# Optimization experiments

Measured on AMD Instinct MI355X. Metric: run time of the kernel, lower is better.

Reference implementation:

```python
import jax, jax.numpy as jnp
import numpy as np

B, L, D, H, T = 1024, 50, 4, 512, 30


def _lstm_cell(x, h, c, W_ih, W_hh, b_ih, b_hh):
    # PyTorch LSTM gate order: i, f, g, o
    g = x @ W_ih.T + b_ih + h @ W_hh.T + b_hh
    i, f, gg, o = jnp.split(g, 4, axis=-1)
    c = jax.nn.sigmoid(f) * c + jax.nn.sigmoid(i) * jnp.tanh(gg)
    h = jax.nn.sigmoid(o) * jnp.tanh(c)
    return h, c


def setup_inputs() -> dict:
    key = jax.random.key(0)
    ks = jax.random.split(key, 16)
    s = 0.05
    return {
        "input_tensor": jax.random.normal(ks[0], (B, L, D), jnp.float32),
        "target_len": T,
        "enc_W_ih": jax.random.normal(ks[1], (4 * H, D), jnp.float32) * s,
        "enc_W_hh": jax.random.normal(ks[2], (4 * H, H), jnp.float32) * s,
        "enc_b_ih": jax.random.normal(ks[3], (4 * H,), jnp.float32) * s,
        "enc_b_hh": jax.random.normal(ks[4], (4 * H,), jnp.float32) * s,
        "attn_W": jax.random.normal(ks[5], (L, H + D), jnp.float32) * s,
        "attn_b": jax.random.normal(ks[6], (L,), jnp.float32) * s,
        "comb_W": jax.random.normal(ks[7], (H, H + D), jnp.float32) * s,
        "comb_b": jax.random.normal(ks[8], (H,), jnp.float32) * s,
        "dec_W_ih": jax.random.normal(ks[9], (4 * H, H), jnp.float32) * s,
        "dec_W_hh": jax.random.normal(ks[10], (4 * H, H), jnp.float32) * s,
        "dec_b_ih": jax.random.normal(ks[11], (4 * H,), jnp.float32) * s,
        "dec_b_hh": jax.random.normal(ks[12], (4 * H,), jnp.float32) * s,
        "out_W": jax.random.normal(ks[13], (D, H), jnp.float32) * s,
        "out_b": jax.random.normal(ks[14], (D,), jnp.float32) * s,
    }


def reference(input_tensor, target_len, enc_W_ih, enc_W_hh, enc_b_ih, enc_b_hh,
              attn_W, attn_b, comb_W, comb_b,
              dec_W_ih, dec_W_hh, dec_b_ih, dec_b_hh, out_W, out_b):
    b = input_tensor.shape[0]

    # ---- encoder LSTM over input_len steps ----
    def enc_step(carry, x_t):
        h, c = carry
        h, c = _lstm_cell(x_t, h, c, enc_W_ih, enc_W_hh, enc_b_ih, enc_b_hh)
        return (h, c), h

    h0 = jnp.zeros((b, H), input_tensor.dtype)
    (h_enc, c_enc), enc_hs = jax.lax.scan(enc_step, (h0, h0),
                                          jnp.swapaxes(input_tensor, 0, 1))
    encoder_outputs = jnp.swapaxes(enc_hs, 0, 1)  # [B, L, H]

    # ---- recursive attention decoder over target_len steps ----
    def dec_step(carry, _):
        h, c, x = carry
        # faithful to torch: h.reshape(h.shape[1], -1).transpose(1, 0)
        h_r = jnp.transpose(h.reshape(H, -1))  # [B, H] (memory reinterpret)
        attn_logits = jnp.concatenate([x, h_r], axis=1) @ attn_W.T + attn_b
        attn_weights = jax.nn.softmax(attn_logits, axis=1)        # [B, L]
        attn_applied = jnp.einsum('bl,blh->bh', attn_weights, encoder_outputs)
        comb = jnp.concatenate([x, attn_applied], axis=1) @ comb_W.T + comb_b
        comb = jax.nn.relu(comb)                                  # [B, H]
        h, c = _lstm_cell(comb, h, c, dec_W_ih, dec_W_hh, dec_b_ih, dec_b_hh)
        pred = h @ out_W.T + out_b                                # [B, D]
        return (h, c, pred), pred

    dec_in0 = input_tensor[:, -1, :]
    _, preds = jax.lax.scan(dec_step, (h_enc, c_enc, dec_in0), None,
                            length=target_len)
    return jnp.swapaxes(preds, 0, 1)  # [B, target_len, D]
```

## Files before the change

kernel.cpp:

```cpp
#include <hip/hip_runtime.h>
#include <hip/hip_bf16.h>

#define Bsz   1024
#define Lseq  50
#define Din   4
#define Hd    512
#define Tlen  30
#define NWG   256

typedef __hip_bfloat16 bf16;
typedef short s16x8 __attribute__((ext_vector_type(8)));
typedef short s16x4 __attribute__((ext_vector_type(4)));
typedef float f32x4 __attribute__((ext_vector_type(4)));
typedef int   i32x2 __attribute__((ext_vector_type(2)));

__device__ __forceinline__ float bf2f(bf16 x){ return __bfloat162float(x); }
__device__ __forceinline__ bf16  f2bf(float x){ return __float2bfloat16(x); }
__device__ __forceinline__ float bfbits2f(short u){
    union { unsigned int ui; float f; } v;
    v.ui = ((unsigned int)(unsigned short)u) << 16;
    return v.f;
}
__device__ __forceinline__ short f2bfbits(float x){
    bf16 h = f2bf(x); short s; __builtin_memcpy(&s, &h, 2); return s;
}
__device__ __forceinline__ float sigm(float x){ return 1.0f/(1.0f + __expf(-x)); }
__device__ __forceinline__ float ftanh(float x){
    const float e = __expf(2.0f*x);
    return 1.0f - 2.0f/(e + 1.0f);
}
__device__ __forceinline__ i32x2 pack4(float a, float b, float c, float d){
    i32x2 v;
    v[0] = (int)(unsigned short)f2bfbits(a) | ((int)(unsigned short)f2bfbits(b) << 16);
    v[1] = (int)(unsigned short)f2bfbits(c) | ((int)(unsigned short)f2bfbits(d) << 16);
    return v;
}

#define OFF_ABUF0   (0u)
#define OFF_ABUF1   (2u<<20)
#define OFF_ATTNAP  (8u<<20)
#define OFF_XDEC    (9u<<20)
#define OFF_FLAG    ((9u<<20) + (16u<<10))
#define OFF_COMBWR  ((9u<<20) + (32u<<10))
#define OFF_ATTNWR  ((9u<<20) + (600u<<10))
#define OFF_FLAGS   ((9u<<20) + (704u<<10))
#define OFF_WCACHE  (10u<<20)
#define OFF_ENCOUT  (18u<<20)

#define WC_INPUT 0
#define WC_EWIH  204800
#define WC_EWHH  212992
#define WC_EBIH  1261568
#define WC_EBHH  1263616
#define WC_AW    1265664
#define WC_AB    1291464
#define WC_CW    1291520
#define WC_CB    1555712
#define WC_DWIH  1556224
#define WC_DWHH  2604800
#define WC_DBIH  3653376
#define WC_DBHH  3655424
#define WC_OW    3657472
#define WC_OB    3659520
#define WC_TOTAL 3659524

__device__ __constant__ int WOFF[15] = {
    WC_INPUT, WC_EWIH, WC_EWHH, WC_EBIH, WC_EBHH, WC_AW, WC_AB, WC_CW,
    WC_CB, WC_DWIH, WC_DWHH, WC_DBIH, WC_DBHH, WC_OW, WC_OB };
__device__ __constant__ int WNUM[15] = {
    204800, 8192, 1048576, 2048, 2048, 25800, 50, 264192,
    512, 1048576, 1048576, 2048, 2048, 2048, 4 };

struct Ptrs15 { const void* p[15]; };

__global__ void probe_kernel(const unsigned int* __restrict__ w, int* flag){
    __shared__ int cnt;
    if (threadIdx.x == 0) cnt = 0;
    __syncthreads();
    int c = 0;
    for (int i = threadIdx.x; i < 4096; i += 256){
        unsigned e = (w[i] >> 7) & 0xFFu;
        c += (e >= 0x80u) ? 1 : 0;
    }
    atomicAdd(&cnt, c);
    __syncthreads();
    if (threadIdx.x == 0) *flag = (cnt > 400) ? 1 : 0;
}

__global__ __launch_bounds__(256) void convert_kernel(
    Ptrs15 srcs, const int* __restrict__ flag, bf16* __restrict__ dst)
{
    const int f = *flag;
    for (int idx = blockIdx.x*256 + threadIdx.x; idx < WC_TOTAL;
         idx += gridDim.x*256){
        int a = 0;
#pragma unroll
        for (int j = 1; j < 15; ++j) if (idx >= WOFF[j]) a = j;
        const int local = idx - WOFF[a];
        if (local >= WNUM[a]) continue;
        bf16 v;
        if (f) v = f2bf(((const float*)srcs.p[a])[local]);
        else   v = ((const bf16*)srcs.p[a])[local];
        dst[idx] = v;
    }
}

__global__ __launch_bounds__(256) void setup_kernel(
    bf16* __restrict__ Abuf0, bf16* __restrict__ Abuf1,
    bf16* __restrict__ combWr, bf16* __restrict__ attnWr,
    const bf16* __restrict__ cWc, const bf16* __restrict__ aWc)
{
    const unsigned idx = blockIdx.x*256u + threadIdx.x;
    if (idx < (unsigned)Bsz*Hd){
        const unsigned row = idx >> 9, col = idx & (Hd-1);
        const bf16 z = f2bf(0.0f);
        Abuf0[(size_t)row*1024 + Hd + col] = z;
        Abuf1[(size_t)row*1024 + Hd + col] = z;
    }
    if (idx < (unsigned)Hd*Hd)
        combWr[idx] = cWc[(size_t)(idx >> 9)*(Hd+Din) + Din + (idx & (Hd-1))];
    if (idx < (unsigned)Lseq*Hd)
        attnWr[idx] = aWc[(size_t)(idx >> 9)*(Hd+Din) + Din + (idx & (Hd-1))];
}

struct MegaP {
    const bf16 *input, *eWih, *eWhh, *ebih, *ebhh;
    const bf16 *aW, *ab, *cW, *cb, *dWih, *dWhh, *dbih, *dbhh, *oW, *ob;
    const bf16 *combWr, *attnWr;
    bf16 *A0, *A1, *encout, *attnap, *xdec;
    int *wflag, *gflag, *xccmap;
    const int *flag;
    void *dout;
};

__global__ __launch_bounds__(512, 2) void mega_kernel(MegaP P)
{
    __shared__ short whh_lds[128*536];
    __shared__ short hr_s[4][Hd];
    __shared__ float ctx_s[2][4][8][64];
    __shared__ float aw_s[4][64];
    __shared__ int   xmap_s[NWG];
    __shared__ int   info_s[2];

    const int wg = blockIdx.x, tid = threadIdx.x;
    const int wave = tid >> 6, lane = tid & 63;
    const int quad = lane >> 4, l15 = lane & 15;
    const int lbase = lane & ~3;
    const int f32out = *P.flag;

    const int grp = wg & 7, rank = wg >> 3;

    int ep = 0;

    auto flag_round = [&](bool fence){
        ++ep;
        __syncthreads();
        if (tid == 0){
            if (fence) __threadfence();
            __hip_atomic_store(P.wflag + wg*16, ep, __ATOMIC_RELAXED, __HIP_MEMORY_SCOPE_SYSTEM);
        }
        if (rank == 0){
            if (tid < 32){
                int* f = P.wflag + (tid*8 + grp)*16;
                while (__hip_atomic_load(f, __ATOMIC_RELAXED, __HIP_MEMORY_SCOPE_SYSTEM) < ep)
                    __builtin_amdgcn_s_sleep(1);
            }
            __syncthreads();
            if (tid == 0)
                __hip_atomic_store(P.gflag + grp*16, ep, __ATOMIC_RELAXED, __HIP_MEMORY_SCOPE_SYSTEM);
        }
        if (tid < 8){
            int* f = P.gflag + tid*16;
            while (__hip_atomic_load(f, __ATOMIC_RELAXED, __HIP_MEMORY_SCOPE_SYSTEM) < ep)
                __builtin_amdgcn_s_sleep(1);
        }
        __syncthreads();
    };

    auto GSYNC = [&](){
        flag_round(true);
        asm volatile("buffer_inv sc0 sc1" ::: "memory");
        __syncthreads();
        flag_round(false);
    };

    auto XSYNC = [&](int balv){
        if (!balv){ GSYNC(); return; }
        ++ep;
        __syncthreads();
        if (tid == 0)
            __hip_atomic_store(P.wflag + wg*16, ep, __ATOMIC_RELAXED, __HIP_MEMORY_SCOPE_SYSTEM);
        if (tid < 32){
            int* f = P.wflag + (tid*8 + grp)*16;
            while (__hip_atomic_load(f, __ATOMIC_RELAXED, __HIP_MEMORY_SCOPE_SYSTEM) < ep)
                __builtin_amdgcn_s_sleep(1);
        }
        __syncthreads();
        asm volatile("buffer_inv" ::: "memory");
    };

    if (tid == 0){
        int xcc = 0;
        asm volatile("s_getreg_b32 %0, hwreg(HW_REG_XCC_ID)" : "=s"(xcc));
        P.xccmap[wg] = xcc & 7;
    }
    GSYNC();
    if (tid < NWG) xmap_s[tid] = P.xccmap[tid];
    __syncthreads();
    if (tid == 0){
        int ok = 1;
        for (int g = 0; g < 8; ++g){
            const int x0 = xmap_s[g];
            for (int i = 1; i < 32; ++i) ok &= (xmap_s[i*8 + g] == x0);
        }
        info_s[0] = ok;
    }
    __syncthreads();
    const int bal = info_s[0];

    bf16* bufs[2] = { P.A0, P.A1 };

    const int mt = grp*2 + (rank >> 4), nt = rank & 15;
    const int bm0 = mt << 6, hc0 = nt << 5;
    const int wm = wave >> 2, wn = wave & 3;
    const int arow0 = bm0 + wm*32 + l15;

    int ng[2];
#pragma unroll
    for (int nf = 0; nf < 2; ++nf){
        const int n = wn*32 + nf*16 + l15;
        ng[nf] = (n & 3)*Hd + hc0 + (n >> 2);
    }

    float bias_e[2], wxv_e[2][4];
#pragma unroll
    for (int nf = 0; nf < 2; ++nf){
        bias_e[nf] = bf2f(P.ebih[ng[nf]]) + bf2f(P.ebhh[ng[nf]]);
        const s16x4 t4 = *reinterpret_cast<const s16x4*>(P.eWih + (size_t)ng[nf]*Din);
#pragma unroll
        for (int d = 0; d < 4; ++d) wxv_e[nf][d] = bfbits2f(t4[d]);
    }

    s16x8 breg[2][16];
#pragma unroll
    for (int nf = 0; nf < 2; ++nf)
#pragma unroll
        for (int sl = 0; sl < 16; ++sl)
            breg[nf][sl] = *reinterpret_cast<const s16x8*>(
                P.eWhh + (size_t)ng[nf]*Hd + sl*32 + quad*8);

    float creg[2][2][4];
#pragma unroll
    for (int a = 0; a < 2; ++a)
#pragma unroll
        for (int b = 0; b < 2; ++b)
#pragma unroll
            for (int r = 0; r < 4; ++r) creg[a][b][r] = 0.0f;

    for (int t = 0; t < Lseq; ++t){
        const bf16* Ain = bufs[t&1] + Hd;
        bf16* hout = bufs[(t+1)&1] + Hd;

        f32x4 acc[2][2];
#pragma unroll
        for (int mf=0; mf<2; ++mf)
#pragma unroll
            for (int nf=0; nf<2; ++nf) acc[mf][nf] = (f32x4)0.0f;

        s16x8 afr[2];
#pragma unroll
        for (int sl = 0; sl < 16; ++sl){
#pragma unroll
            for (int mf = 0; mf < 2; ++mf)
                afr[mf] = *reinterpret_cast<const s16x8*>(
                    Ain + (size_t)(arow0 + mf*16)*1024 + sl*32 + quad*8);
#pragma unroll
            for (int mf = 0; mf < 2; ++mf)
#pragma unroll
                for (int nf = 0; nf < 2; ++nf)
                    acc[mf][nf] = __builtin_amdgcn_mfma_f32_16x16x32_bf16(
                        afr[mf], breg[nf][sl], acc[mf][nf], 0, 0, 0);
        }

#pragma unroll
        for (int mf = 0; mf < 2; ++mf){
#pragma unroll
            for (int r = 0; r < 4; ++r){
                const int m = bm0 + wm*32 + mf*16 + quad*4 + r;
                const s16x4 xt = *reinterpret_cast<const s16x4*>(
                    P.input + ((size_t)m*Lseq + t)*Din);
                float xv[4];
#pragma unroll
                for (int d = 0; d < 4; ++d) xv[d] = bfbits2f(xt[d]);
#pragma unroll
                for (int nf = 0; nf < 2; ++nf){
                    const int n_loc = wn*32 + nf*16 + l15;
                    float gv = acc[mf][nf][r] + bias_e[nf]
                             + xv[0]*wxv_e[nf][0] + xv[1]*wxv_e[nf][1]
                             + xv[2]*wxv_e[nf][2] + xv[3]*wxv_e[nf][3];
                    const float gi = __shfl(gv, lbase+0);
                    const float gf = __shfl(gv, lbase+1);
                    const float gg = __shfl(gv, lbase+2);
                    const float go = __shfl(gv, lbase+3);
                    if ((lane & 3) == 0){
                        const int hcol = hc0 + (n_loc >> 2);
                        const float cn = sigm(gf)*creg[mf][nf][r] + sigm(gi)*ftanh(gg);
                        creg[mf][nf][r] = cn;
                        const float hv = sigm(go)*ftanh(cn);
                        const bf16 hb = f2bf(hv);
                        hout[(size_t)m*1024 + hcol] = hb;
                        P.encout[((size_t)m*Lseq + t)*Hd + hcol] = hb;
                    }
                }
            }
        }
        if (t == Lseq-1) GSYNC(); else XSYNC(bal);
    }

#pragma unroll
    for (int nf = 0; nf < 2; ++nf)
#pragma unroll
        for (int sl = 0; sl < 16; ++sl)
            breg[nf][sl] = *reinterpret_cast<const s16x8*>(
                P.dWih + (size_t)ng[nf]*Hd + sl*32 + quad*8);

    float bias_d[2];
#pragma unroll
    for (int nf = 0; nf < 2; ++nf)
        bias_d[nf] = bf2f(P.dbih[ng[nf]]) + bf2f(P.dbhh[ng[nf]]);

    for (int i = tid; i < 128*64; i += 512){
        const int col = i >> 6;
        const int k8  = (i & 63) * 8;
        const int g   = (col & 3)*Hd + hc0 + (col >> 2);
        const s16x8 v = *reinterpret_cast<const s16x8*>(P.dWhh + (size_t)g*Hd + k8);
        *reinterpret_cast<s16x8*>(&whh_lds[col*536 + k8]) = v;
    }

    const int b0 = grp*128 + rank*4;
    const int s_uni = b0 >> 9;
    const int p0 = b0 & (Hd-1);

    const int cwm = wave >> 1, cwn = wave & 1;
    const int ccol = hc0 + cwn*16 + l15;
    float bias_c, wxv_c[4];
    {
        bias_c = bf2f(P.cb[ccol]);
        const s16x4 t4 = *reinterpret_cast<const s16x4*>(P.cW + (size_t)ccol*(Hd+Din));
#pragma unroll
        for (int d = 0; d < 4; ++d) wxv_c[d] = bfbits2f(t4[d]);
    }
    __syncthreads();

    for (int t = 0; t < Tlen; ++t){
        const int p = t & 1;
        const bf16* hprev = bufs[p] + Hd;

        {
            const s16x4 hv = *reinterpret_cast<const s16x4*>(
                hprev + (size_t)(2*tid + s_uni)*1024 + p0);
            hr_s[0][tid] = hv[0]; hr_s[1][tid] = hv[1];
            hr_s[2][tid] = hv[2]; hr_s[3][tid] = hv[3];
        }
        __syncthreads();

        if (wave < 4){
            const int b = b0 + wave;
            float x0, x1, x2, x3;
            if (t == 0){
                const bf16* xp = P.input + ((size_t)b*Lseq + (Lseq-1))*Din;
                x0 = bf2f(xp[0]); x1 = bf2f(xp[1]); x2 = bf2f(xp[2]); x3 = bf2f(xp[3]);
            } else {
                float q0=0.f, q1=0.f, q2=0.f, q3=0.f;
                const bf16* hb = hprev + (size_t)b*1024;
                for (int k = lane; k < Hd; k += 64){
                    const float hv = bf2f(hb[k]);
                    q0 += hv*bf2f(P.oW[k]);
                    q1 += hv*bf2f(P.oW[Hd+k]);
                    q2 += hv*bf2f(P.oW[2*Hd+k]);
                    q3 += hv*bf2f(P.oW[3*Hd+k]);
                }
#pragma unroll
                for (int off = 32; off; off >>= 1){
                    q0 += __shfl_down(q0, off); q1 += __shfl_down(q1, off);
                    q2 += __shfl_down(q2, off); q3 += __shfl_down(q3, off);
                }
                x0 = __shfl(q0,0) + bf2f(P.ob[0]);
                x1 = __shfl(q1,0) + bf2f(P.ob[1]);
                x2 = __shfl(q2,0) + bf2f(P.ob[2]);
                x3 = __shfl(q3,0) + bf2f(P.ob[3]);
                if (lane == 0){
                    const size_t o = ((size_t)b*Tlen + (t-1))*Din;
                    if (f32out){
                        float* dp = (float*)P.dout + o;
                        dp[0]=x0; dp[1]=x1; dp[2]=x2; dp[3]=x3;
                    } else {
                        *reinterpret_cast<i32x2*>((bf16*)P.dout + o) = pack4(x0,x1,x2,x3);
                    }
                }
            }
            if (lane == 0)
                *reinterpret_cast<i32x2*>(P.xdec + (size_t)b*Din) = pack4(x0,x1,x2,x3);

            float logit = -3.0e38f;
            if (lane < Lseq){
                float a0 = bf2f(P.ab[lane]);
                {
                    const bf16* wx = P.aW + (size_t)lane*(Hd+Din);
                    a0 += x0*bf2f(wx[0]) + x1*bf2f(wx[1]) + x2*bf2f(wx[2]) + x3*bf2f(wx[3]);
                }
                float a1 = 0.f, a2 = 0.f, a3 = 0.f;
                const bf16* wr = P.attnWr + (size_t)lane*Hd;
                for (int j = 0; j < Hd; j += 16){
                    float t4[4] = {0.f,0.f,0.f,0.f};
#pragma unroll
                    for (int q = 0; q < 4; ++q){
                        const s16x4 hw = *reinterpret_cast<const s16x4*>(&hr_s[wave][j + q*4]);
                        const s16x4 wv = *reinterpret_cast<const s16x4*>(wr + j + q*4);
                        t4[q] = bfbits2f(hw[0])*bfbits2f(wv[0]) + bfbits2f(hw[1])*bfbits2f(wv[1])
                              + bfbits2f(hw[2])*bfbits2f(wv[2]) + bfbits2f(hw[3])*bfbits2f(wv[3]);
                    }
                    a0 += t4[0]; a1 += t4[1]; a2 += t4[2]; a3 += t4[3];
                }
                logit = (a0 + a1) + (a2 + a3);
            }
            float mx = logit;
#pragma unroll
            for (int off = 32; off; off >>= 1) mx = fmaxf(mx, __shfl_xor(mx, off));
            const float e = (lane < Lseq) ? __expf(logit - mx) : 0.0f;
            float se = e;
#pragma unroll
            for (int off = 32; off; off >>= 1) se += __shfl_xor(se, off);
            aw_s[wave][lane] = e / se;
        }
        __syncthreads();

        {
            const int r = wave & 3, half = wave >> 2;
            const int b = b0 + r;
            float acc8[8] = {0.f,0.f,0.f,0.f,0.f,0.f,0.f,0.f};
            const bf16* eb = P.encout + (size_t)b*Lseq*Hd + lane*8;
            for (int i = 0; i < 25; ++i){
                const int l = half*25 + i;
                const float w = aw_s[r][l];
                const s16x8 ch = *reinterpret_cast<const s16x8*>(eb + (size_t)l*Hd);
#pragma unroll
                for (int q = 0; q < 8; ++q) acc8[q] += w * bfbits2f(ch[q]);
            }
#pragma unroll
            for (int q = 0; q < 8; ++q) ctx_s[half][r][q][lane] = acc8[q];
        }
        __syncthreads();

        if (wave < 4){
            const int b = b0 + wave;
            s16x8 ov;
#pragma unroll
            for (int q = 0; q < 8; ++q)
                ov[q] = f2bfbits(ctx_s[0][wave][q][lane] + ctx_s[1][wave][q][lane]);
            *reinterpret_cast<s16x8*>(P.attnap + (size_t)b*Hd + lane*8) = ov;
        }
        XSYNC(bal);

        {
            f32x4 cacc = (f32x4)0.0f;
            const bf16* Ab = P.attnap + (size_t)(bm0 + cwm*16 + l15)*Hd + quad*8;
#pragma unroll
            for (int kk = 0; kk < 16; ++kk){
                const s16x8 bfr = *reinterpret_cast<const s16x8*>(
                    P.combWr + (size_t)ccol*Hd + kk*32 + quad*8);
                const s16x8 afr2 = *reinterpret_cast<const s16x8*>(Ab + kk*32);
                cacc = __builtin_amdgcn_mfma_f32_16x16x32_bf16(afr2, bfr, cacc, 0, 0, 0);
            }
            bf16* outp = bufs[p];
#pragma unroll
            for (int r = 0; r < 4; ++r){
                const int m = bm0 + cwm*16 + quad*4 + r;
                const s16x4 xt = *reinterpret_cast<const s16x4*>(P.xdec + (size_t)m*Din);
                float v = cacc[r] + bias_c
                        + bfbits2f(xt[0])*wxv_c[0] + bfbits2f(xt[1])*wxv_c[1]
                        + bfbits2f(xt[2])*wxv_c[2] + bfbits2f(xt[3])*wxv_c[3];
                v = fmaxf(v, 0.0f);
                outp[(size_t)m*1024 + ccol] = f2bf(v);
            }
        }
        XSYNC(bal);

        {
            const bf16* Ain = bufs[p];
            bf16* hout = bufs[p^1] + Hd;
            f32x4 acc[2][2];
#pragma unroll
            for (int mf=0; mf<2; ++mf)
#pragma unroll
                for (int nf=0; nf<2; ++nf) acc[mf][nf] = (f32x4)0.0f;

            s16x8 afr[2], bfr[2];
#pragma unroll
            for (int sl = 0; sl < 16; ++sl){
#pragma unroll
                for (int mf = 0; mf < 2; ++mf)
                    afr[mf] = *reinterpret_cast<const s16x8*>(
                        Ain + (size_t)(arow0 + mf*16)*1024 + sl*32 + quad*8);
#pragma unroll
                for (int mf = 0; mf < 2; ++mf)
#pragma unroll
                    for (int nf = 0; nf < 2; ++nf)
                        acc[mf][nf] = __builtin_amdgcn_mfma_f32_16x16x32_bf16(
                            afr[mf], breg[nf][sl], acc[mf][nf], 0, 0, 0);
            }
#pragma unroll
            for (int sl = 0; sl < 16; ++sl){
#pragma unroll
                for (int nf = 0; nf < 2; ++nf){
                    const int nl = wn*32 + nf*16 + l15;
                    bfr[nf] = *reinterpret_cast<const s16x8*>(
                        &whh_lds[nl*536 + sl*32 + quad*8]);
                }
#pragma unroll
                for (int mf = 0; mf < 2; ++mf)
                    afr[mf] = *reinterpret_cast<const s16x8*>(
                        Ain + (size_t)(arow0 + mf*16)*1024 + Hd + sl*32 + quad*8);
#pragma unroll
                for (int mf = 0; mf < 2; ++mf)
#pragma unroll
                    for (int nf = 0; nf < 2; ++nf)
                        acc[mf][nf] = __builtin_amdgcn_mfma_f32_16x16x32_bf16(
                            afr[mf], bfr[nf], acc[mf][nf], 0, 0, 0);
            }

#pragma unroll
            for (int mf = 0; mf < 2; ++mf){
#pragma unroll
                for (int r = 0; r < 4; ++r){
                    const int m = bm0 + wm*32 + mf*16 + quad*4 + r;
#pragma unroll
                    for (int nf = 0; nf < 2; ++nf){
                        const int n_loc = wn*32 + nf*16 + l15;
                        float gv = acc[mf][nf][r] + bias_d[nf];
                        const float gi = __shfl(gv, lbase+0);
                        const float gf = __shfl(gv, lbase+1);
                        const float gg = __shfl(gv, lbase+2);
                        const float go = __shfl(gv, lbase+3);
                        if ((lane & 3) == 0){
                            const int hcol = hc0 + (n_loc >> 2);
                            const float cn = sigm(gf)*creg[mf][nf][r] + sigm(gi)*ftanh(gg);
                            creg[mf][nf][r] = cn;
                            const float hv = sigm(go)*ftanh(cn);
                            hout[(size_t)m*1024 + hcol] = f2bf(hv);
                        }
                    }
                }
            }
        }
        GSYNC();
    }

    if (wave < 4){
        const int b = b0 + wave;
        const bf16* hb = bufs[Tlen & 1] + Hd + (size_t)b*1024;
        float q0=0.f, q1=0.f, q2=0.f, q3=0.f;
        for (int k = lane; k < Hd; k += 64){
            const float hv = bf2f(hb[k]);
            q0 += hv*bf2f(P.oW[k]);
            q1 += hv*bf2f(P.oW[Hd+k]);
            q2 += hv*bf2f(P.oW[2*Hd+k]);
            q3 += hv*bf2f(P.oW[3*Hd+k]);
        }
#pragma unroll
        for (int off = 32; off; off >>= 1){
            q0 += __shfl_down(q0, off); q1 += __shfl_down(q1, off);
            q2 += __shfl_down(q2, off); q3 += __shfl_down(q3, off);
        }
        if (lane == 0){
            const size_t o = ((size_t)b*Tlen + (Tlen-1))*Din;
            const float r0 = q0 + bf2f(P.ob[0]), r1 = q1 + bf2f(P.ob[1]);
            const float r2 = q2 + bf2f(P.ob[2]), r3 = q3 + bf2f(P.ob[3]);
            if (f32out){
                float* dp = (float*)P.dout + o;
                dp[0]=r0; dp[1]=r1; dp[2]=r2; dp[3]=r3;
            } else {
                *reinterpret_cast<i32x2*>((bf16*)P.dout + o) = pack4(r0,r1,r2,r3);
            }
        }
    }
}

extern "C" void kernel_launch(void* const* d_in, const int* in_sizes, int n_in,
                              void* d_out, int out_size, void* d_ws, size_t ws_size,
                              hipStream_t stream)
{
    char* ws = (char*)d_ws;
    bf16*  Abuf0   = (bf16*)(ws + OFF_ABUF0);
    bf16*  Abuf1   = (bf16*)(ws + OFF_ABUF1);
    bf16*  attnap  = (bf16*)(ws + OFF_ATTNAP);
    bf16*  xdec    = (bf16*)(ws + OFF_XDEC);
    int*   flag    = (int*)(ws + OFF_FLAG);
    bf16*  combWr  = (bf16*)(ws + OFF_COMBWR);
    bf16*  attnWr  = (bf16*)(ws + OFF_ATTNWR);
    int*   flags   = (int*)(ws + OFF_FLAGS);
    bf16*  wc      = (bf16*)(ws + OFF_WCACHE);
    bf16*  enc_out = (bf16*)(ws + OFF_ENCOUT);

    hipMemsetAsync(flags, 0, 20480, stream);

    probe_kernel<<<1, 256, 0, stream>>>((const unsigned int*)d_in[3], flag);

    Ptrs15 srcs;
    srcs.p[0]=d_in[0];  srcs.p[1]=d_in[2];  srcs.p[2]=d_in[3];  srcs.p[3]=d_in[4];
    srcs.p[4]=d_in[5];  srcs.p[5]=d_in[6];  srcs.p[6]=d_in[7];  srcs.p[7]=d_in[8];
    srcs.p[8]=d_in[9];  srcs.p[9]=d_in[10]; srcs.p[10]=d_in[11];srcs.p[11]=d_in[12];
    srcs.p[12]=d_in[13];srcs.p[13]=d_in[14];srcs.p[14]=d_in[15];
    convert_kernel<<<1024, 256, 0, stream>>>(srcs, flag, wc);

    setup_kernel<<<2048, 256, 0, stream>>>(Abuf0, Abuf1, combWr, attnWr,
                                           wc+WC_CW, wc+WC_AW);

    MegaP P;
    P.input = wc+WC_INPUT; P.eWih = wc+WC_EWIH; P.eWhh = wc+WC_EWHH;
    P.ebih = wc+WC_EBIH;   P.ebhh = wc+WC_EBHH;
    P.aW = wc+WC_AW;  P.ab = wc+WC_AB;  P.cW = wc+WC_CW;  P.cb = wc+WC_CB;
    P.dWih = wc+WC_DWIH; P.dWhh = wc+WC_DWHH; P.dbih = wc+WC_DBIH; P.dbhh = wc+WC_DBHH;
    P.oW = wc+WC_OW;  P.ob = wc+WC_OB;
    P.combWr = combWr; P.attnWr = attnWr;
    P.A0 = Abuf0; P.A1 = Abuf1; P.encout = enc_out; P.attnap = attnap; P.xdec = xdec;
    P.wflag = flags; P.gflag = flags + 256*16; P.xccmap = flags + 256*16 + 8*16;
    P.flag = flag; P.dout = d_out;

    mega_kernel<<<NWG, 512, 0, stream>>>(P);
}
```

Measured before the change: 3.850 ms.

## Retile per-XCC batch slabs, move weights to LDS, cache encoder outputs in registers

Changes the work split so each workgroup owns 128 batch rows and 16 hidden columns, keeping each batch slab within one XCC group. Both decoder weight matrices and the encoder Whh now live in LDS instead of registers. Encoder outputs are preloaded into registers for the attention context, and the global syncs become single-round local-cache invalidations when the XCC placement is balanced. It also adds a system-coherent load for the reinterpreted hidden state. This aims to cut sync latency and cross-XCC traffic, at the cost of LDS bandwidth on every MFMA step and correctness that now relies on the balanced XCC placement.

New measurement: 3.504 ms. 1.1x faster.

```diff
diff --git a/kernel.cpp b/kernel.cpp
--- a/kernel.cpp
+++ b/kernel.cpp
@@ -34,6 +34,12 @@
     v[0] = (int)(unsigned short)f2bfbits(a) | ((int)(unsigned short)f2bfbits(b) << 16);
     v[1] = (int)(unsigned short)f2bfbits(c) | ((int)(unsigned short)f2bfbits(d) << 16);
     return v;
+}
+__device__ __forceinline__ s16x4 sc_load_b64(const void* p){
+    i32x2 v;
+    asm volatile("global_load_dwordx2 %0, %1, off sc0 sc1\n\ts_waitcnt vmcnt(0)"
+                 : "=v"(v) : "v"(p) : "memory");
+    s16x4 r; __builtin_memcpy(&r, &v, 8); return r;
 }
 
 #define OFF_ABUF0   (0u)
@@ -133,9 +139,12 @@
     void *dout;
 };
 
+#define WSTRIDE 536
+
 __global__ __launch_bounds__(512, 2) void mega_kernel(MegaP P)
 {
-    __shared__ short whh_lds[128*536];
+    __shared__ short w1_lds[64*WSTRIDE];
+    __shared__ short w2_lds[64*WSTRIDE];
     __shared__ short hr_s[4][Hd];
     __shared__ float ctx_s[2][4][8][64];
     __shared__ float aw_s[4][64];
@@ -177,26 +186,10 @@
         __syncthreads();
     };
 
-    auto GSYNC = [&](){
+    auto GSYNCF = [&](){
         flag_round(true);
         asm volatile("buffer_inv sc0 sc1" ::: "memory");
         __syncthreads();
-        flag_round(false);
-    };
-
-    auto XSYNC = [&](int balv){
-        if (!balv){ GSYNC(); return; }
-        ++ep;
-        __syncthreads();
-        if (tid == 0)
-            __hip_atomic_store(P.wflag + wg*16, ep, __ATOMIC_RELAXED, __HIP_MEMORY_SCOPE_SYSTEM);
-        if (tid < 32){
-            int* f = P.wflag + (tid*8 + grp)*16;
-            while (__hip_atomic_load(f, __ATOMIC_RELAXED, __HIP_MEMORY_SCOPE_SYSTEM) < ep)
-                __builtin_amdgcn_s_sleep(1);
-        }
-        __syncthreads();
-        asm volatile("buffer_inv" ::: "memory");
     };
 
     if (tid == 0){
@@ -204,7 +197,7 @@
         asm volatile("s_getreg_b32 %0, hwreg(HW_REG_XCC_ID)" : "=s"(xcc));
         P.xccmap[wg] = xcc & 7;
     }
-    GSYNC();
+    GSYNCF();
     if (tid < NWG) xmap_s[tid] = P.xccmap[tid];
     __syncthreads();
     if (tid == 0){
@@ -218,11 +211,31 @@
     __syncthreads();
     const int bal = info_s[0];
 
+    auto GSYNCL = [&](){
+        if (!bal){ GSYNCF(); return; }
+        flag_round(true);
+        asm volatile("buffer_inv" ::: "memory");
+        __syncthreads();
+    };
+    auto XSYNC = [&](){
+        if (!bal){ GSYNCF(); return; }
+        ++ep;
+        __syncthreads();
+        if (tid == 0)
+            __hip_atomic_store(P.wflag + wg*16, ep, __ATOMIC_RELAXED, __HIP_MEMORY_SCOPE_SYSTEM);
+        if (tid < 32){
+            int* f = P.wflag + (tid*8 + grp)*16;
+            while (__hip_atomic_load(f, __ATOMIC_RELAXED, __HIP_MEMORY_SCOPE_SYSTEM) < ep)
+                __builtin_amdgcn_s_sleep(1);
+        }
+        __syncthreads();
+        asm volatile("buffer_inv" ::: "memory");
+    };
+
     bf16* bufs[2] = { P.A0, P.A1 };
 
-    const int mt = grp*2 + (rank >> 4), nt = rank & 15;
-    const int bm0 = mt << 6, hc0 = nt << 5;
-    const int wm = wave >> 2, wn = wave & 3;
+    const int bm0 = grp*128, hc0 = rank*16;
+    const int wm = wave >> 1, wn = wave & 1;
     const int arow0 = bm0 + wm*32 + l15;
 
     int ng[2];
@@ -241,13 +254,13 @@
         for (int d = 0; d < 4; ++d) wxv_e[nf][d] = bfbits2f(t4[d]);
     }
 
-    s16x8 breg[2][16];
-#pragma unroll
-    for (int nf = 0; nf < 2; ++nf)
-#pragma unroll
-        for (int sl = 0; sl < 16; ++sl)
-            breg[nf][sl] = *reinterpret_cast<const s16x8*>(
-                P.eWhh + (size_t)ng[nf]*Hd + sl*32 + quad*8);
+    for (int i = tid; i < 64*64; i += 512){
+        const int col = i >> 6, k8 = (i & 63)*8;
+        const int g = (col & 3)*Hd + hc0 + (col >> 2);
+        const s16x8 v = *reinterpret_cast<const s16x8*>(P.eWhh + (size_t)g*Hd + k8);
+        *reinterpret_cast<s16x8*>(&w2_lds[col*WSTRIDE + k8]) = v;
+    }
+    __syncthreads();
 
     float creg[2][2][4];
 #pragma unroll
@@ -267,7 +280,7 @@
 #pragma unroll
             for (int nf=0; nf<2; ++nf) acc[mf][nf] = (f32x4)0.0f;
 
-        s16x8 afr[2];
+        s16x8 afr[2], bfr[2];
 #pragma unroll
         for (int sl = 0; sl < 16; ++sl){
 #pragma unroll
@@ -275,11 +288,17 @@
                 afr[mf] = *reinterpret_cast<const s16x8*>(
                     Ain + (size_t)(arow0 + mf*16)*1024 + sl*32 + quad*8);
 #pragma unroll
+            for (int nf = 0; nf < 2; ++nf){
+                const int nl = wn*32 + nf*16 + l15;
+                bfr[nf] = *reinterpret_cast<const s16x8*>(
+                    &w2_lds[nl*WSTRIDE + sl*32 + quad*8]);
+            }
+#pragma unroll
             for (int mf = 0; mf < 2; ++mf)
 #pragma unroll
                 for (int nf = 0; nf < 2; ++nf)
                     acc[mf][nf] = __builtin_amdgcn_mfma_f32_16x16x32_bf16(
-                        afr[mf], breg[nf][sl], acc[mf][nf], 0, 0, 0);
+                        afr[mf], bfr[nf], acc[mf][nf], 0, 0, 0);
         }
 
 #pragma unroll
@@ -314,35 +333,37 @@
                 }
             }
         }
-        if (t == Lseq-1) GSYNC(); else XSYNC(bal);
-    }
-
-#pragma unroll
-    for (int nf = 0; nf < 2; ++nf)
-#pragma unroll
-        for (int sl = 0; sl < 16; ++sl)
-            breg[nf][sl] = *reinterpret_cast<const s16x8*>(
-                P.dWih + (size_t)ng[nf]*Hd + sl*32 + quad*8);
+        if (t == Lseq-1) GSYNCL(); else XSYNC();
+    }
+
+    for (int i = tid; i < 64*64; i += 512){
+        const int col = i >> 6, k8 = (i & 63)*8;
+        const int g = (col & 3)*Hd + hc0 + (col >> 2);
+        *reinterpret_cast<s16x8*>(&w1_lds[col*WSTRIDE + k8]) =
+            *reinterpret_cast<const s16x8*>(P.dWih + (size_t)g*Hd + k8);
+        *reinterpret_cast<s16x8*>(&w2_lds[col*WSTRIDE + k8]) =
+            *reinterpret_cast<const s16x8*>(P.dWhh + (size_t)g*Hd + k8);
+    }
 
     float bias_d[2];
 #pragma unroll
     for (int nf = 0; nf < 2; ++nf)
         bias_d[nf] = bf2f(P.dbih[ng[nf]]) + bf2f(P.dbhh[ng[nf]]);
-
-    for (int i = tid; i < 128*64; i += 512){
-        const int col = i >> 6;
-        const int k8  = (i & 63) * 8;
-        const int g   = (col & 3)*Hd + hc0 + (col >> 2);
-        const s16x8 v = *reinterpret_cast<const s16x8*>(P.dWhh + (size_t)g*Hd + k8);
-        *reinterpret_cast<s16x8*>(&whh_lds[col*536 + k8]) = v;
-    }
 
     const int b0 = grp*128 + rank*4;
     const int s_uni = b0 >> 9;
     const int p0 = b0 & (Hd-1);
 
-    const int cwm = wave >> 1, cwn = wave & 1;
-    const int ccol = hc0 + cwn*16 + l15;
+    const int rr = wave & 3, half = wave >> 2;
+    s16x8 ereg[25];
+    {
+        const bf16* eb = P.encout + (size_t)(b0 + rr)*Lseq*Hd + lane*8;
+#pragma unroll
+        for (int i = 0; i < 25; ++i)
+            ereg[i] = *reinterpret_cast<const s16x8*>(eb + (size_t)(half*25 + i)*Hd);
+    }
+
+    const int ccol = hc0 + l15;
     float bias_c, wxv_c[4];
     {
         bias_c = bf2f(P.cb[ccol]);
@@ -357,8 +378,7 @@
         const bf16* hprev = bufs[p] + Hd;
 
         {
-            const s16x4 hv = *reinterpret_cast<const s16x4*>(
-                hprev + (size_t)(2*tid + s_uni)*1024 + p0);
+            const s16x4 hv = sc_load_b64(hprev + (size_t)(2*tid + s_uni)*1024 + p0);
             hr_s[0][tid] = hv[0]; hr_s[1][tid] = hv[1];
             hr_s[2][tid] = hv[2]; hr_s[3][tid] = hv[3];
         }
@@ -436,19 +456,15 @@
         __syncthreads();
 
         {
-            const int r = wave & 3, half = wave >> 2;
-            const int b = b0 + r;
             float acc8[8] = {0.f,0.f,0.f,0.f,0.f,0.f,0.f,0.f};
-            const bf16* eb = P.encout + (size_t)b*Lseq*Hd + lane*8;
+#pragma unroll
             for (int i = 0; i < 25; ++i){
-                const int l = half*25 + i;
-                const float w = aw_s[r][l];
-                const s16x8 ch = *reinterpret_cast<const s16x8*>(eb + (size_t)l*Hd);
-#pragma unroll
-                for (int q = 0; q < 8; ++q) acc8[q] += w * bfbits2f(ch[q]);
-            }
-#pragma unroll
-            for (int q = 0; q < 8; ++q) ctx_s[half][r][q][lane] = acc8[q];
+                const float w = aw_s[rr][half*25 + i];
+#pragma unroll
+                for (int q = 0; q < 8; ++q) acc8[q] += w * bfbits2f(ereg[i][q]);
+            }
+#pragma unroll
+            for (int q = 0; q < 8; ++q) ctx_s[half][rr][q][lane] = acc8[q];
         }
         __syncthreads();
 
@@ -460,11 +476,11 @@
                 ov[q] = f2bfbits(ctx_s[0][wave][q][lane] + ctx_s[1][wave][q][lane]);
             *reinterpret_cast<s16x8*>(P.attnap + (size_t)b*Hd + lane*8) = ov;
         }
-        XSYNC(bal);
+        XSYNC();
 
         {
             f32x4 cacc = (f32x4)0.0f;
-            const bf16* Ab = P.attnap + (size_t)(bm0 + cwm*16 + l15)*Hd + quad*8;
+            const bf16* Ab = P.attnap + (size_t)(bm0 + wave*16 + l15)*Hd + quad*8;
 #pragma unroll
             for (int kk = 0; kk < 16; ++kk){
                 const s16x8 bfr = *reinterpret_cast<const s16x8*>(
@@ -475,7 +491,7 @@
             bf16* outp = bufs[p];
 #pragma unroll
             for (int r = 0; r < 4; ++r){
-                const int m = bm0 + cwm*16 + quad*4 + r;
+                const int m = bm0 + wave*16 + quad*4 + r;
                 const s16x4 xt = *reinterpret_cast<const s16x4*>(P.xdec + (size_t)m*Din);
                 float v = cacc[r] + bias_c
                         + bfbits2f(xt[0])*wxv_c[0] + bfbits2f(xt[1])*wxv_c[1]
@@ -484,7 +500,7 @@
                 outp[(size_t)m*1024 + ccol] = f2bf(v);
             }
         }
-        XSYNC(bal);
+        XSYNC();
 
         {
             const bf16* Ain = bufs[p];
@@ -503,24 +519,30 @@
                     afr[mf] = *reinterpret_cast<const s16x8*>(
                         Ain + (size_t)(arow0 + mf*16)*1024 + sl*32 + quad*8);
 #pragma unroll
-                for (int mf = 0; mf < 2; ++mf)
-#pragma unroll
-                    for (int nf = 0; nf < 2; ++nf)
-                        acc[mf][nf] = __builtin_amdgcn_mfma_f32_16x16x32_bf16(
-                            afr[mf], breg[nf][sl], acc[mf][nf], 0, 0, 0);
-            }
-#pragma unroll
-            for (int sl = 0; sl < 16; ++sl){
-#pragma unroll
                 for (int nf = 0; nf < 2; ++nf){
                     const int nl = wn*32 + nf*16 + l15;
                     bfr[nf] = *reinterpret_cast<const s16x8*>(
-                        &whh_lds[nl*536 + sl*32 + quad*8]);
-                }
+                        &w1_lds[nl*WSTRIDE + sl*32 + quad*8]);
+                }
+#pragma unroll
+                for (int mf = 0; mf < 2; ++mf)
+#pragma unroll
+                    for (int nf = 0; nf < 2; ++nf)
+                        acc[mf][nf] = __builtin_amdgcn_mfma_f32_16x16x32_bf16(
+                            afr[mf], bfr[nf], acc[mf][nf], 0, 0, 0);
+            }
+#pragma unroll
+            for (int sl = 0; sl < 16; ++sl){
 #pragma unroll
                 for (int mf = 0; mf < 2; ++mf)
                     afr[mf] = *reinterpret_cast<const s16x8*>(
                         Ain + (size_t)(arow0 + mf*16)*1024 + Hd + sl*32 + quad*8);
+#pragma unroll
+                for (int nf = 0; nf < 2; ++nf){
+                    const int nl = wn*32 + nf*16 + l15;
+                    bfr[nf] = *reinterpret_cast<const s16x8*>(
+                        &w2_lds[nl*WSTRIDE + sl*32 + quad*8]);
+                }
 #pragma unroll
                 for (int mf = 0; mf < 2; ++mf)
 #pragma unroll
@@ -553,7 +575,7 @@
                 }
             }
         }
-        GSYNC();
+        GSYNCL();
     }
 
     if (wave < 4){
```
